# Optimization experiments

Measured on AMD Instinct MI355X. Metric: run time of the kernel, lower is better.

The kernel has to match this reference:

```python
import jax, jax.numpy as jnp
import numpy as np

B, T, F, H, O = 256, 128, 128, 1024, 128


def setup_inputs() -> dict:
    key = jax.random.key(0)
    ks = jax.random.split(key, 16)
    s = 0.02  # small init scale to keep gates in a sane range
    return {
        "batch": jax.random.normal(ks[0], (B, T, F), jnp.float32),
        "Wih0": jax.random.normal(ks[1], (4 * H, F), jnp.float32) * s,
        "Whh0": jax.random.normal(ks[2], (4 * H, H), jnp.float32) * s,
        "bih0": jax.random.normal(ks[3], (4 * H,), jnp.float32) * s,
        "bhh0": jax.random.normal(ks[4], (4 * H,), jnp.float32) * s,
        "Wih1": jax.random.normal(ks[5], (4 * H, H), jnp.float32) * s,
        "Whh1": jax.random.normal(ks[6], (4 * H, H), jnp.float32) * s,
        "bih1": jax.random.normal(ks[7], (4 * H,), jnp.float32) * s,
        "bhh1": jax.random.normal(ks[8], (4 * H,), jnp.float32) * s,
        "h00": jax.random.normal(ks[9], (B, H), jnp.float32) * s,
        "c00": jax.random.normal(ks[10], (B, H), jnp.float32) * s,
        "h01": jax.random.normal(ks[11], (B, H), jnp.float32) * s,
        "c01": jax.random.normal(ks[12], (B, H), jnp.float32) * s,
        "Wout": jax.random.normal(ks[13], (O, T * H), jnp.float32) * 0.01,
        "bout": jax.random.normal(ks[14], (O,), jnp.float32) * 0.01,
    }


def _lstm_cell(x, h, c, Wih, Whh, bih, bhh):
    # torch.nn.LSTMCell: gates = x @ Wih.T + bih + h @ Whh.T + bhh, chunks i,f,g,o
    gates = x @ Wih.T + bih + h @ Whh.T + bhh  # [B, 4H]
    i, f, g, o = jnp.split(gates, 4, axis=-1)
    c_new = jax.nn.sigmoid(f) * c + jax.nn.sigmoid(i) * jnp.tanh(g)
    h_new = jax.nn.sigmoid(o) * jnp.tanh(c_new)
    return h_new, c_new


def reference(batch, Wih0, Whh0, bih0, bhh0, Wih1, Whh1, bih1, bhh1,
              h00, c00, h01, c01, Wout, bout):
    # Faithful to original: batch.view(T, B, -1) is a pure RESHAPE, not transpose.
    x = batch.reshape(T, B, F)

    def step(carry, xt):
        h0, c0, h1, c1 = carry
        h0, c0 = _lstm_cell(xt, h0, c0, Wih0, Whh0, bih0, bhh0)
        h1, c1 = _lstm_cell(h0, h1, c1, Wih1, Whh1, bih1, bhh1)
        return (h0, c0, h1, c1), h1

    _, outs = jax.lax.scan(step, (h00, c00, h01, c01), x)  # outs: [T, B, H]
    # Faithful: io.view(B, T, -1) then Flatten -> pure reshape to [B, T*H]
    flat = outs.reshape(B, T * H)
    return flat @ Wout.T + bout  # [B, O]
```

## Files before the change

### kernel.cpp

```cpp
#include <hip/hip_runtime.h>
#include <hip/hip_cooperative_groups.h>

namespace cg = cooperative_groups;

typedef __attribute__((ext_vector_type(8))) short short8;
typedef __attribute__((ext_vector_type(4))) float f32x4;

#define NBATCH 256
#define NSTEP  128
#define NFEAT  128
#define NHID   1024
#define NOUT   128
#define KOUT   131072
#define NBLK   256

#define W0H_OFF 0
#define W1_OFF  32768
#define CH_OFF  98304
#define SMEM_BYTES 163840

#define CTR_STRIDE 272
#define CTR_TOTAL  (129 * CTR_STRIDE)

#define MFMA __builtin_amdgcn_mfma_f32_16x16x32_bf16

__device__ __forceinline__ unsigned short f2bf(float f){
  unsigned u = __float_as_uint(f);
  u += 0x7fffu + ((u >> 16) & 1u);
  return (unsigned short)(u >> 16);
}
__device__ __forceinline__ float sigf(float x){
  x = fminf(fmaxf(x, -30.f), 30.f);
  return 1.f / (1.f + __expf(-x));
}
__device__ __forceinline__ float tanhf_(float x){
  x = fminf(fmaxf(x, -15.f), 15.f);
  float e = __expf(2.f * x);
  return (e - 1.f) / (e + 1.f);
}

struct Params {
  const float *batch,*Wih0,*Whh0,*bih0,*bhh0,*Wih1,*Whh1,*bih1,*bhh1,*h00,*c00,*h01,*c01,*Wout,*bout;
  float *out;
  unsigned short *h0b,*h1b,*outs,*xbf;
  float *partial;
  unsigned *ctr;
};

__device__ __forceinline__ short8 ld8(const unsigned short* p){
  return *(const short8*)p;
}
__device__ __forceinline__ short8 ld8f(const float* p){
  f32x4 a = *(const f32x4*)p;
  f32x4 b = *(const f32x4*)(p + 4);
  short8 r;
  r[0]=(short)f2bf(a[0]); r[1]=(short)f2bf(a[1]); r[2]=(short)f2bf(a[2]); r[3]=(short)f2bf(a[3]);
  r[4]=(short)f2bf(b[0]); r[5]=(short)f2bf(b[1]); r[6]=(short)f2bf(b[2]); r[7]=(short)f2bf(b[3]);
  return r;
}

__device__ __forceinline__ void dma16(const void* g, void* l){
  __builtin_amdgcn_global_load_lds((const __attribute__((address_space(1))) unsigned int*)g,
                                   (__attribute__((address_space(3))) unsigned int*)l, 16, 0, 0);
}

__device__ __forceinline__ unsigned long long pack4(unsigned short u){
  unsigned v = (unsigned)u | ((unsigned)(unsigned short)__shfl_xor((int)(unsigned)u, 16) << 16);
  unsigned hi32 = (unsigned)__shfl_xor((int)v, 32);
  return (unsigned long long)v | ((unsigned long long)hi32 << 32);
}
__device__ __forceinline__ void st8a(unsigned short* p, unsigned long long v){
  __hip_atomic_store((unsigned long long*)p, v, __ATOMIC_RELAXED, __HIP_MEMORY_SCOPE_AGENT);
}

__device__ __forceinline__ void tree_bar(unsigned* base, int bx, int tid){
  asm volatile("s_waitcnt vmcnt(0)" ::: "memory");
  __syncthreads();
  if (tid == 0) {
    unsigned old = __hip_atomic_fetch_add(base + (bx & 15) * 16, 1u,
                                          __ATOMIC_RELAXED, __HIP_MEMORY_SCOPE_AGENT);
    if (old == 15u)
      __hip_atomic_fetch_add(base + 256, 1u, __ATOMIC_RELAXED, __HIP_MEMORY_SCOPE_AGENT);
    while (__hip_atomic_load(base + 256, __ATOMIC_RELAXED, __HIP_MEMORY_SCOPE_AGENT) < 16u)
      __builtin_amdgcn_s_sleep(1);
  }
  __syncthreads();
  __builtin_amdgcn_fence(__ATOMIC_ACQUIRE, "agent");
}

__global__ void __launch_bounds__(512, 2) lstm_all(Params a)
{
  extern __shared__ char smem[];
  const int bx = blockIdx.x, tid = threadIdx.x;
  const int gtid = bx * 512 + tid, nthr = gridDim.x * 512;
  const int w = tid >> 6, l = tid & 63, lo = l & 15, hi = l >> 4;
  const int klane = hi * 8;
  const int dR  = l >> 2;
  const int dgo = (((l & 3) ^ ((l >> 3) & 3)) & 3) * 8;

  for (int i = gtid; i < CTR_TOTAL; i += nthr) a.ctr[i] = 0;
  for (int item = tid; item < 128 * 16; item += 512) {
    int g = item >> 4, lr = item & 15;
    int r = 16 * bx + lr, orig = (r & 3) * NHID + (r >> 2);
    *(short8*)(smem + W0H_OFF + item * 16) = ld8f(a.Whh0 + (size_t)orig * NHID + g * 8);
  }
  for (int item = tid; item < 256 * 16; item += 512) {
    int g = item >> 4, lr = item & 15;
    int r = 16 * bx + lr, orig = (r & 3) * NHID + (r >> 2);
    int k = g * 8;
    const float* src = (k < NHID) ? a.Wih1 + (size_t)orig * NHID + k
                                  : a.Whh1 + (size_t)orig * NHID + (k - NHID);
    *(short8*)(smem + W1_OFF + item * 16) = ld8f(src);
  }
  short8 wx[4];
  {
    int r = 16 * bx + lo, orig = (r & 3) * NHID + (r >> 2);
    const float* s = a.Wih0 + (size_t)orig * NFEAT + klane;
    #pragma unroll
    for (int i = 0; i < 4; i++) wx[i] = ld8f(s + i * 32);
  }
  for (int i = gtid; i < NBATCH * NHID; i += nthr) {
    a.h0b[NBATCH * NHID + i] = f2bf(a.h00[i]);
    a.h1b[NBATCH * NHID + i] = f2bf(a.h01[i]);
  }
  for (int i = gtid; i < NSTEP * NBATCH * NFEAT / 8; i += nthr)
    *(short8*)(a.xbf + (size_t)i * 8) = ld8f(a.batch + (size_t)i * 8);

  const int j = 4 * bx + hi;
  float b0r[4], b1r[4];
  #pragma unroll
  for (int q = 0; q < 4; q++) {
    b0r[q] = a.bih0[q * NHID + j] + a.bhh0[q * NHID + j];
    b1r[q] = a.bih1[q * NHID + j] + a.bhh1[q * NHID + j];
  }
  const int m0 = w * 32 + lo, m1 = m0 + 16;
  float c0r[2], c1r[2];
  c0r[0] = a.c00[(size_t)m0 * NHID + j]; c0r[1] = a.c00[(size_t)m1 * NHID + j];
  c1r[0] = a.c01[(size_t)m0 * NHID + j]; c1r[1] = a.c01[(size_t)m1 * NHID + j];
  __syncthreads();
  cg::this_grid().sync();

  const int rdo = lo * 64 + ((hi ^ ((lo >> 1) & 3)) << 4);
  for (int p = 0; p <= NSTEP; p++) {
    const int wpar = p & 1, rp = wpar ^ 1;
    const unsigned short* h0p = a.h0b + (size_t)rp   * NBATCH * NHID;
    const unsigned short* h1p = a.h1b + (size_t)wpar * NBATCH * NHID;
    const int t0 = (p < NSTEP) ? p : (NSTEP - 1);
    const unsigned short* xA  = a.xbf + (size_t)t0 * NBATCH * NFEAT + (size_t)(w * 32 + dR) * NFEAT + dgo;
    const unsigned short* h0A = h0p + (size_t)(w * 32 + dR) * NHID + dgo;
    const unsigned short* h1A = h1p + (size_t)(w * 32 + dR) * NHID + dgo;

    auto issue = [&](int cc){
      char* base = smem + CH_OFF + (cc & 3) * 16384 + w * 2048;
      if (cc < 4) {
        int ko = cc * 32;
        dma16(xA + ko, base); dma16(xA + 16 * NFEAT + ko, base + 1024);
      } else if (cc < 36) {
        int ko = (cc - 4) * 32;
        dma16(h0A + ko, base); dma16(h0A + 16 * NHID + ko, base + 1024);
      } else {
        int ko = (cc - 36) * 32;
        dma16(h1A + ko, base); dma16(h1A + 16 * NHID + ko, base + 1024);
      }
    };

    f32x4 l0a0 = {0.f,0.f,0.f,0.f}, l0a1 = {0.f,0.f,0.f,0.f};
    f32x4 l1a0 = {0.f,0.f,0.f,0.f}, l1a1 = {0.f,0.f,0.f,0.f};

    issue(0); issue(1); issue(2);

    #pragma unroll
    for (int c = 0; c < 68; ++c) {
      if      (c <= 65) asm volatile("s_waitcnt vmcnt(4)\n\ts_barrier" ::: "memory");
      else if (c == 66) asm volatile("s_waitcnt vmcnt(2)\n\ts_barrier" ::: "memory");
      else              asm volatile("s_waitcnt vmcnt(0)\n\ts_barrier" ::: "memory");
      if (c + 3 < 68) issue(c + 3);

      const char* cb = smem + CH_OFF + (c & 3) * 16384 + w * 2048;
      short8 a0 = *(const short8*)(cb + rdo);
      short8 a1 = *(const short8*)(cb + 1024 + rdo);

      if (c < 4) {
        l0a0 = MFMA(wx[c], a0, l0a0, 0,0,0); l0a1 = MFMA(wx[c], a1, l0a1, 0,0,0);
      } else if (c < 36) {
        int g = (c - 4) * 4 + hi;
        short8 w0f = *(const short8*)(smem + W0H_OFF + g * 256 + lo * 16);
        short8 w1f = *(const short8*)(smem + W1_OFF  + g * 256 + lo * 16);
        l0a0 = MFMA(w0f, a0, l0a0, 0,0,0); l0a1 = MFMA(w0f, a1, l0a1, 0,0,0);
        l1a0 = MFMA(w1f, a0, l1a0, 0,0,0); l1a1 = MFMA(w1f, a1, l1a1, 0,0,0);
      } else {
        int g = 128 + (c - 36) * 4 + hi;
        short8 wf = *(const short8*)(smem + W1_OFF + g * 256 + lo * 16);
        l1a0 = MFMA(wf, a0, l1a0, 0,0,0); l1a1 = MFMA(wf, a1, l1a1, 0,0,0);
      }
    }

    if (p < NSTEP) {
      unsigned short* ho = a.h0b + (size_t)wpar * NBATCH * NHID;
      float cn0 = sigf(l0a0[1] + b0r[1]) * c0r[0] + sigf(l0a0[0] + b0r[0]) * tanhf_(l0a0[2] + b0r[2]);
      c0r[0] = cn0;
      unsigned short hb0 = f2bf(sigf(l0a0[3] + b0r[3]) * tanhf_(cn0));
      float cn1 = sigf(l0a1[1] + b0r[1]) * c0r[1] + sigf(l0a1[0] + b0r[0]) * tanhf_(l0a1[2] + b0r[2]);
      c0r[1] = cn1;
      unsigned short hb1 = f2bf(sigf(l0a1[3] + b0r[3]) * tanhf_(cn1));
      unsigned long long pk0 = pack4(hb0), pk1 = pack4(hb1);
      if (hi == 0) {
        st8a(ho + (size_t)m0 * NHID + 4 * bx, pk0);
        st8a(ho + (size_t)m1 * NHID + 4 * bx, pk1);
      }
    }
    if (p >= 1) {
      unsigned short* h1o = a.h1b + (size_t)rp * NBATCH * NHID;
      unsigned short* oo  = a.outs + (size_t)(p - 1) * NBATCH * NHID;
      float cn0 = sigf(l1a0[1] + b1r[1]) * c1r[0] + sigf(l1a0[0] + b1r[0]) * tanhf_(l1a0[2] + b1r[2]);
      c1r[0] = cn0;
      unsigned short hb0 = f2bf(sigf(l1a0[3] + b1r[3]) * tanhf_(cn0));
      float cn1 = sigf(l1a1[1] + b1r[1]) * c1r[1] + sigf(l1a1[0] + b1r[0]) * tanhf_(l1a1[2] + b1r[2]);
      c1r[1] = cn1;
      unsigned short hb1 = f2bf(sigf(l1a1[3] + b1r[3]) * tanhf_(cn1));
      unsigned long long pk0 = pack4(hb0), pk1 = pack4(hb1);
      if (hi == 0) {
        st8a(h1o + (size_t)m0 * NHID + 4 * bx, pk0);
        st8a(h1o + (size_t)m1 * NHID + 4 * bx, pk1);
        st8a(oo  + (size_t)m0 * NHID + 4 * bx, pk0);
        st8a(oo  + (size_t)m1 * NHID + 4 * bx, pk1);
      }
    }
    tree_bar(a.ctr + p * CTR_STRIDE, bx, tid);
  }

  cg::this_grid().sync();

  {
    int fnt = bx & 3, kc = bx >> 2;
    f32x4 facc[2][2];
    #pragma unroll
    for (int i = 0; i < 2; i++) { facc[i][0] = (f32x4)(0.f); facc[i][1] = (f32x4)(0.f); }
    const int kbase = kc * 2048;
    #pragma unroll 2
    for (int kk = 0; kk < 64; kk++) {
      short8 wf0 = ld8f(a.Wout + (size_t)(fnt * 32 +  0 + lo) * KOUT + kbase + kk * 32 + klane);
      short8 wf1 = ld8f(a.Wout + (size_t)(fnt * 32 + 16 + lo) * KOUT + kbase + kk * 32 + klane);
      #pragma unroll
      for (int mf = 0; mf < 2; mf++) {
        const unsigned short* ip = a.outs + (size_t)((w * 2 + mf) * 16 + lo) * KOUT + kbase + kk * 32 + klane;
        short8 af = ld8(ip);
        facc[mf][0] = MFMA(wf0, af, facc[mf][0], 0,0,0);
        facc[mf][1] = MFMA(wf1, af, facc[mf][1], 0,0,0);
      }
    }
    #pragma unroll
    for (int mf = 0; mf < 2; mf++)
      #pragma unroll
      for (int nf = 0; nf < 2; nf++)
        #pragma unroll
        for (int r = 0; r < 4; r++) {
          int o_loc = nf * 16 + 4 * hi + r;
          int i = (w * 2 + mf) * 16 + lo;
          a.partial[(size_t)(kc * 4 + fnt) * 8192 + o_loc * 256 + i] = facc[mf][nf][r];
        }
  }
  cg::this_grid().sync();

  for (int idx = gtid; idx < NBATCH * NOUT; idx += nthr) {
    int i = idx >> 7, o = idx & 127;
    float s = a.bout[o];
    #pragma unroll 4
    for (int kc2 = 0; kc2 < 64; kc2++)
      s += a.partial[(size_t)(kc2 * 4 + (o >> 5)) * 8192 + (o & 31) * 256 + i];
    a.out[idx] = s;
  }
}

extern "C" void kernel_launch(void* const* d_in, const int* in_sizes, int n_in,
                              void* d_out, int out_size, void* d_ws, size_t ws_size,
                              hipStream_t stream)
{
  (void)in_sizes; (void)n_in; (void)out_size; (void)ws_size;
  Params a;
  a.batch = (const float*)d_in[0];  a.Wih0 = (const float*)d_in[1];
  a.Whh0  = (const float*)d_in[2];  a.bih0 = (const float*)d_in[3];
  a.bhh0  = (const float*)d_in[4];  a.Wih1 = (const float*)d_in[5];
  a.Whh1  = (const float*)d_in[6];  a.bih1 = (const float*)d_in[7];
  a.bhh1  = (const float*)d_in[8];  a.h00  = (const float*)d_in[9];
  a.c00   = (const float*)d_in[10]; a.h01  = (const float*)d_in[11];
  a.c01   = (const float*)d_in[12]; a.Wout = (const float*)d_in[13];
  a.bout  = (const float*)d_in[14];
  a.out   = (float*)d_out;

  char* ws = (char*)d_ws;
  size_t off = 0;
  auto carve = [&](size_t bytes) { char* p = ws + off; off += (bytes + 255) & ~(size_t)255; return p; };
  a.h0b     = (unsigned short*)carve((size_t)2 * NBATCH * NHID * 2);
  a.h1b     = (unsigned short*)carve((size_t)2 * NBATCH * NHID * 2);
  a.outs    = (unsigned short*)carve((size_t)NSTEP * NBATCH * NHID * 2);
  a.xbf     = (unsigned short*)carve((size_t)NSTEP * NBATCH * NFEAT * 2);
  a.partial = (float*)carve((size_t)256 * 8192 * 4);
  a.ctr     = (unsigned*)carve((size_t)CTR_TOTAL * 4);

  hipFuncSetAttribute((const void*)lstm_all, hipFuncAttributeMaxDynamicSharedMemorySize, SMEM_BYTES);

  void* kargs[] = { &a };
  hipLaunchCooperativeKernel((void*)lstm_all, dim3(256), dim3(512), kargs, SMEM_BYTES, stream);
}
```

Before: 4.991 ms.

## Hold first half of recurrent weights in registers and deepen chunk prefetch to six

The first 16 K-chunks of Whh0 and Wih1 now live in per-lane registers instead of LDS, so those steps do no LDS weight reads. The freed LDS space lets the activation staging ring grow from four to six buffers, so five chunks are in flight instead of three, with waitcnt thresholds adjusted to match. This is meant to hide global/L2 latency on the per-step h reloads and cut LDS traffic. It adds 32 short8 registers per lane, which may hurt occupancy under the 2-blocks launch bound or cause spills.

```diff
diff --git a/kernel.cpp b/kernel.cpp
--- a/kernel.cpp
+++ b/kernel.cpp
@@ -15,8 +15,8 @@
 #define NBLK   256
 
 #define W0H_OFF 0
-#define W1_OFF  32768
-#define CH_OFF  98304
+#define W1_OFF  16384
+#define CH_OFF  65536
 #define SMEM_BYTES 163840
 
 #define CTR_STRIDE 272
@@ -99,25 +99,31 @@
   const int dgo = (((l & 3) ^ ((l >> 3) & 3)) & 3) * 8;
 
   for (int i = gtid; i < CTR_TOTAL; i += nthr) a.ctr[i] = 0;
-  for (int item = tid; item < 128 * 16; item += 512) {
-    int g = item >> 4, lr = item & 15;
+  for (int item = tid; item < 64 * 16; item += 512) {
+    int gp = item >> 4, lr = item & 15;
     int r = 16 * bx + lr, orig = (r & 3) * NHID + (r >> 2);
-    *(short8*)(smem + W0H_OFF + item * 16) = ld8f(a.Whh0 + (size_t)orig * NHID + g * 8);
-  }
-  for (int item = tid; item < 256 * 16; item += 512) {
-    int g = item >> 4, lr = item & 15;
+    *(short8*)(smem + W0H_OFF + item * 16) = ld8f(a.Whh0 + (size_t)orig * NHID + (64 + gp) * 8);
+  }
+  for (int item = tid; item < 192 * 16; item += 512) {
+    int gp = item >> 4, lr = item & 15;
     int r = 16 * bx + lr, orig = (r & 3) * NHID + (r >> 2);
-    int k = g * 8;
-    const float* src = (k < NHID) ? a.Wih1 + (size_t)orig * NHID + k
-                                  : a.Whh1 + (size_t)orig * NHID + (k - NHID);
+    int g = 64 + gp;
+    const float* src = (g < 128) ? a.Wih1 + (size_t)orig * NHID + g * 8
+                                 : a.Whh1 + (size_t)orig * NHID + (g - 128) * 8;
     *(short8*)(smem + W1_OFF + item * 16) = ld8f(src);
   }
-  short8 wx[4];
+  short8 wx[4], w0r[16], w1r[16];
   {
     int r = 16 * bx + lo, orig = (r & 3) * NHID + (r >> 2);
-    const float* s = a.Wih0 + (size_t)orig * NFEAT + klane;
-    #pragma unroll
-    for (int i = 0; i < 4; i++) wx[i] = ld8f(s + i * 32);
+    const float* sx = a.Wih0 + (size_t)orig * NFEAT + klane;
+    #pragma unroll
+    for (int i = 0; i < 4; i++) wx[i] = ld8f(sx + i * 32);
+    const float* s0 = a.Whh0 + (size_t)orig * NHID + klane;
+    #pragma unroll
+    for (int i = 0; i < 16; i++) w0r[i] = ld8f(s0 + i * 32);
+    const float* s1 = a.Wih1 + (size_t)orig * NHID + klane;
+    #pragma unroll
+    for (int i = 0; i < 16; i++) w1r[i] = ld8f(s1 + i * 32);
   }
   for (int i = gtid; i < NBATCH * NHID; i += nthr) {
     a.h0b[NBATCH * NHID + i] = f2bf(a.h00[i]);
@@ -151,7 +157,7 @@
     const unsigned short* h1A = h1p + (size_t)(w * 32 + dR) * NHID + dgo;
 
     auto issue = [&](int cc){
-      char* base = smem + CH_OFF + (cc & 3) * 16384 + w * 2048;
+      char* base = smem + CH_OFF + (cc % 6) * 16384 + w * 2048;
       if (cc < 4) {
         int ko = cc * 32;
         dma16(xA + ko, base); dma16(xA + 16 * NFEAT + ko, base + 1024);
@@ -167,30 +173,35 @@
     f32x4 l0a0 = {0.f,0.f,0.f,0.f}, l0a1 = {0.f,0.f,0.f,0.f};
     f32x4 l1a0 = {0.f,0.f,0.f,0.f}, l1a1 = {0.f,0.f,0.f,0.f};
 
-    issue(0); issue(1); issue(2);
+    issue(0); issue(1); issue(2); issue(3); issue(4);
 
     #pragma unroll
     for (int c = 0; c < 68; ++c) {
-      if      (c <= 65) asm volatile("s_waitcnt vmcnt(4)\n\ts_barrier" ::: "memory");
+      if      (c <= 63) asm volatile("s_waitcnt vmcnt(8)\n\ts_barrier" ::: "memory");
+      else if (c == 64) asm volatile("s_waitcnt vmcnt(6)\n\ts_barrier" ::: "memory");
+      else if (c == 65) asm volatile("s_waitcnt vmcnt(4)\n\ts_barrier" ::: "memory");
       else if (c == 66) asm volatile("s_waitcnt vmcnt(2)\n\ts_barrier" ::: "memory");
       else              asm volatile("s_waitcnt vmcnt(0)\n\ts_barrier" ::: "memory");
-      if (c + 3 < 68) issue(c + 3);
-
-      const char* cb = smem + CH_OFF + (c & 3) * 16384 + w * 2048;
+      if (c + 5 < 68) issue(c + 5);
+
+      const char* cb = smem + CH_OFF + (c % 6) * 16384 + w * 2048;
       short8 a0 = *(const short8*)(cb + rdo);
       short8 a1 = *(const short8*)(cb + 1024 + rdo);
 
       if (c < 4) {
         l0a0 = MFMA(wx[c], a0, l0a0, 0,0,0); l0a1 = MFMA(wx[c], a1, l0a1, 0,0,0);
+      } else if (c < 20) {
+        l0a0 = MFMA(w0r[c - 4], a0, l0a0, 0,0,0); l0a1 = MFMA(w0r[c - 4], a1, l0a1, 0,0,0);
+        l1a0 = MFMA(w1r[c - 4], a0, l1a0, 0,0,0); l1a1 = MFMA(w1r[c - 4], a1, l1a1, 0,0,0);
       } else if (c < 36) {
-        int g = (c - 4) * 4 + hi;
-        short8 w0f = *(const short8*)(smem + W0H_OFF + g * 256 + lo * 16);
-        short8 w1f = *(const short8*)(smem + W1_OFF  + g * 256 + lo * 16);
+        int gp = (c - 20) * 4 + hi;
+        short8 w0f = *(const short8*)(smem + W0H_OFF + gp * 256 + lo * 16);
+        short8 w1f = *(const short8*)(smem + W1_OFF  + gp * 256 + lo * 16);
         l0a0 = MFMA(w0f, a0, l0a0, 0,0,0); l0a1 = MFMA(w0f, a1, l0a1, 0,0,0);
         l1a0 = MFMA(w1f, a0, l1a0, 0,0,0); l1a1 = MFMA(w1f, a1, l1a1, 0,0,0);
       } else {
-        int g = 128 + (c - 36) * 4 + hi;
-        short8 wf = *(const short8*)(smem + W1_OFF + g * 256 + lo * 16);
+        int gp = 64 + (c - 36) * 4 + hi;
+        short8 wf = *(const short8*)(smem + W1_OFF + gp * 256 + lo * 16);
         l1a0 = MFMA(wf, a0, l1a0, 0,0,0); l1a1 = MFMA(wf, a1, l1a1, 0,0,0);
       }
     }
```

Result: no change. 5.064 ms (+1.5%).
